# Kernel tuning notes

Hardware: AMD Instinct MI355X
Metric: run time of the kernel (lower is better)

## Reference

```python
import jax, jax.numpy as jnp
import numpy as np

EMBED = 1024
HEADS = 16
DIM_HEAD = EMBED // HEADS
N, L = 4, 2048


def setup_inputs() -> dict:
    key = jax.random.key(0)
    ks = jax.random.split(key, 12)
    s = 0.02
    return {
        "q": jax.random.normal(ks[0], (N, L, EMBED), jnp.float32),
        "k": jax.random.normal(ks[1], (N, L, EMBED), jnp.float32),
        "v": jax.random.normal(ks[2], (N, L, EMBED), jnp.float32),
        "padding_mask": jnp.ones((N, L), dtype=bool),
        "sequence_mask": jnp.zeros((L, L), dtype=bool),
        # Linear(in, out): store weight as [out, in] like torch, bias [out]
        "Wq": jax.random.normal(ks[3], (EMBED, EMBED), jnp.float32) * s,
        "bq": jnp.zeros((EMBED,), jnp.float32),
        "Wk": jax.random.normal(ks[4], (EMBED, EMBED), jnp.float32) * s,
        "bk": jnp.zeros((EMBED,), jnp.float32),
        "Wv": jax.random.normal(ks[5], (EMBED, EMBED), jnp.float32) * s,
        "bv": jnp.zeros((EMBED,), jnp.float32),
        "Wo": jax.random.normal(ks[6], (EMBED, EMBED), jnp.float32) * s,
        "bo": jnp.zeros((EMBED,), jnp.float32),
    }


def reference(q, k, v, padding_mask, sequence_mask, Wq, bq, Wk, bk, Wv, bv, Wo, bo):
    n, lq, _ = q.shape
    lk = k.shape[1]
    # input projections
    qp = (q @ Wq.T + bq).reshape(n, lq, HEADS, DIM_HEAD)
    kp = (k @ Wk.T + bk).reshape(n, lk, HEADS, DIM_HEAD)
    vp = (v @ Wv.T + bv).reshape(n, lk, HEADS, DIM_HEAD)
    # energy: [n, h, lq, lk]
    energy = jnp.einsum('nqhd,nkhd->nhqk', qp, kp)
    attention = jax.nn.softmax(energy / jnp.sqrt(jnp.float32(EMBED)), axis=3)
    # NOTE: the original torch code calls masked_fill (non in-place) and
    # discards the result, so padding_mask / sequence_mask have NO effect.
    # Dropout is also never applied in forward. Replicated faithfully.
    out = jnp.einsum('nhqk,nkhd->nqhd', attention, vp)
    out = out.reshape(n, lq, EMBED)
    return out @ Wo.T + bo
```

## Files before the change

### kernel.cpp

```cpp
#include <hip/hip_runtime.h>
#include <stdint.h>

typedef _Float16 f16;
typedef _Float16 f16x8 __attribute__((ext_vector_type(8)));
typedef _Float16 f16x4 __attribute__((ext_vector_type(4)));
typedef _Float16 f16x2 __attribute__((ext_vector_type(2)));
typedef __fp16 h16x2 __attribute__((ext_vector_type(2)));
typedef float f32x4 __attribute__((ext_vector_type(4)));

__device__ __forceinline__ f32x4 mfma16(f16x8 a, f16x8 b, f32x4 c) {
    return __builtin_amdgcn_mfma_f32_16x16x32_f16(a, b, c, 0, 0, 0);
}

__device__ __forceinline__ void gload16(const f16* g, f16* l) {
    __builtin_amdgcn_global_load_lds(
        (const __attribute__((address_space(1))) uint32_t*)g,
        (__attribute__((address_space(3))) uint32_t*)l, 16, 0, 0);
}

template <bool OUT16, bool BIASROW, bool XN>
__global__ __launch_bounds__(256, 2) void gemm128h(const f16* __restrict__ A,
                                                   const f16* __restrict__ B,
                                                   const float* __restrict__ bias,
                                                   void* __restrict__ Cout, long ldo) {
    __shared__ __align__(16) f16 As[128 * 64];
    __shared__ __align__(16) f16 Bs[128 * 64];
    int tid = threadIdx.x;
    int lane = tid & 63, w = tid >> 6;
    int wm = w & 1, wn = w >> 1;
    int l15 = lane & 15, quad = lane >> 4;
    long m0 = (long)(XN ? blockIdx.y : blockIdx.x) * 128;
    long n0 = (long)(XN ? blockIdx.x : blockIdx.y) * 128;

    int rg = lane >> 3;
    int cg = (lane & 7) ^ rg;
    const f16* ag[4];
    const f16* bg[4];
    f16* al[4];
    f16* bl[4];
#pragma unroll
    for (int t = 0; t < 4; ++t) {
        int rb = (w * 4 + t) * 8;
        ag[t] = A + (m0 + rb + rg) * 1024 + cg * 8;
        bg[t] = B + (n0 + rb + rg) * 1024 + cg * 8;
        al[t] = &As[rb * 64];
        bl[t] = &Bs[rb * 64];
    }

    f32x4 acc[4][4] = {};

    for (int k0 = 0; k0 < 1024; k0 += 64) {
        __syncthreads();
#pragma unroll
        for (int t = 0; t < 4; ++t) {
            gload16(ag[t] + k0, al[t]);
            gload16(bg[t] + k0, bl[t]);
        }
        __syncthreads();
#pragma unroll
        for (int ks = 0; ks < 2; ++ks) {
            int cc = (ks * 4 + quad) ^ (l15 & 7);
            f16x8 af[4], bf[4];
#pragma unroll
            for (int t = 0; t < 4; ++t) {
                af[t] = *(const f16x8*)&As[(wm * 64 + t * 16 + l15) * 64 + cc * 8];
                bf[t] = *(const f16x8*)&Bs[(wn * 64 + t * 16 + l15) * 64 + cc * 8];
            }
#pragma unroll
            for (int i = 0; i < 4; ++i)
#pragma unroll
                for (int j = 0; j < 4; ++j)
                    acc[i][j] = mfma16(af[i], bf[j], acc[i][j]);
        }
    }

#pragma unroll
    for (int i = 0; i < 4; ++i) {
        int mrow = wm * 64 + i * 16 + quad * 4;
#pragma unroll
        for (int j = 0; j < 4; ++j) {
            int ncol = wn * 64 + j * 16 + l15;
            long gn = n0 + ncol;
#pragma unroll
            for (int r = 0; r < 4; ++r) {
                long gm = m0 + mrow + r;
                float v = acc[i][j][r] + (BIASROW ? bias[gm] : bias[gn]);
                if constexpr (OUT16)
                    ((f16*)Cout)[gm * ldo + gn] = (f16)v;
                else
                    ((float*)Cout)[gm * ldo + gn] = v;
            }
        }
    }
}

__global__ __launch_bounds__(256, 2) void attn128(const f16* __restrict__ Qp,
                                                  const f16* __restrict__ Kp,
                                                  const f16* __restrict__ Vt,
                                                  f16* __restrict__ Op) {
    __shared__ __align__(16) f16 Qs[128 * 64];
    __shared__ __align__(16) f16 Ks[2][64 * 64];
    __shared__ __align__(16) f16 Vs[2][64 * 64];
    __shared__ __align__(16) f16 Ps[128 * 64];
    __shared__ float lsi[128];

    int tid = threadIdx.x;
    int lane = tid & 63, w = tid >> 6;
    int l15 = lane & 15, quad = lane >> 4;
    int b = blockIdx.x;
    int xcd = b & 7, slot = b >> 3;
    int nh = xcd * 8 + (slot >> 4);
    int qt = slot & 15;
    int nb = nh >> 4, h = nh & 15;
    long tok0 = (long)nb * 2048;

    int rg = lane >> 3, cg = (lane & 7) ^ rg;

    const f16* qsrc = Qp + (tok0 + qt * 128) * 1024 + h * 64;
#pragma unroll
    for (int t = 0; t < 4; ++t) {
        int rb = w * 32 + t * 8;
        gload16(qsrc + (rb + rg) * 1024 + cg * 8, &Qs[rb * 64]);
    }
    const f16* kbase = Kp + (tok0 + w * 16 + rg) * 1024 + h * 64 + cg * 8;
    const f16* vbase = Vt + ((long)h * 64 + w * 16 + rg) * 8192 + tok0 + cg * 8;
#pragma unroll
    for (int t = 0; t < 2; ++t) {
        gload16(kbase + t * 8 * 1024, &Ks[0][(w * 16 + t * 8) * 64]);
        gload16(vbase + (long)t * 8 * 8192, &Vs[0][(w * 16 + t * 8) * 64]);
    }
    __syncthreads();

    f16x8 qf[2][2];
#pragma unroll
    for (int ks = 0; ks < 2; ++ks) {
        int cc = (ks * 4 + quad) ^ (l15 & 7);
#pragma unroll
        for (int j = 0; j < 2; ++j)
            qf[ks][j] = *(const f16x8*)&Qs[(w * 32 + j * 16 + l15) * 64 + cc * 8];
    }

    f32x4 oacc[2][4] = {};
    float rsum[2] = {0.f, 0.f};

    for (int kt = 0; kt < 32; ++kt) {
        int cur = kt & 1;
        f32x4 sacc[4][2] = {};
#pragma unroll
        for (int ks = 0; ks < 2; ++ks) {
            int cc = (ks * 4 + quad) ^ (l15 & 7);
            f16x8 af[4];
#pragma unroll
            for (int t = 0; t < 4; ++t)
                af[t] = *(const f16x8*)&Ks[cur][(t * 16 + l15) * 64 + cc * 8];
#pragma unroll
            for (int i = 0; i < 4; ++i)
#pragma unroll
                for (int j = 0; j < 2; ++j)
                    sacc[i][j] = mfma16(af[i], qf[ks][j], sacc[i][j]);
        }
        if (kt < 31) {
            int nxt = cur ^ 1;
            const f16* kp2 = kbase + (long)(kt + 1) * 65536;
            const f16* vp2 = vbase + (kt + 1) * 64;
#pragma unroll
            for (int t = 0; t < 2; ++t) {
                gload16(kp2 + t * 8 * 1024, &Ks[nxt][(w * 16 + t * 8) * 64]);
                gload16(vp2 + (long)t * 8 * 8192, &Vs[nxt][(w * 16 + t * 8) * 64]);
            }
        }
#pragma unroll
        for (int i = 0; i < 4; ++i) {
#pragma unroll
            for (int j = 0; j < 2; ++j) {
                float p0 = __expf(sacc[i][j][0] * 0.03125f);
                float p1 = __expf(sacc[i][j][1] * 0.03125f);
                float p2 = __expf(sacc[i][j][2] * 0.03125f);
                float p3 = __expf(sacc[i][j][3] * 0.03125f);
                rsum[j] += (p0 + p1) + (p2 + p3);
                f16x2 lo = __builtin_bit_cast(f16x2, __builtin_amdgcn_cvt_pkrtz(p0, p1));
                f16x2 hi = __builtin_bit_cast(f16x2, __builtin_amdgcn_cvt_pkrtz(p2, p3));
                f16x4 ph;
                ph[0] = lo[0]; ph[1] = lo[1]; ph[2] = hi[0]; ph[3] = hi[1];
                int qrow = w * 32 + j * 16 + l15;
                int kl = i * 16 + quad * 4;
                int c = kl >> 3;
                *(f16x4*)&Ps[qrow * 64 + ((c ^ (qrow & 7)) << 3) + (kl & 7)] = ph;
            }
        }
        __syncthreads();
#pragma unroll
        for (int ks = 0; ks < 2; ++ks) {
            int cc = (ks * 4 + quad) ^ (l15 & 7);
            f16x8 af[2], bf[4];
#pragma unroll
            for (int i = 0; i < 2; ++i)
                af[i] = *(const f16x8*)&Ps[(w * 32 + i * 16 + l15) * 64 + cc * 8];
#pragma unroll
            for (int j = 0; j < 4; ++j)
                bf[j] = *(const f16x8*)&Vs[cur][(j * 16 + l15) * 64 + cc * 8];
#pragma unroll
            for (int i = 0; i < 2; ++i)
#pragma unroll
                for (int j = 0; j < 4; ++j)
                    oacc[i][j] = mfma16(af[i], bf[j], oacc[i][j]);
        }
        __syncthreads();
    }

#pragma unroll
    for (int j = 0; j < 2; ++j) {
        rsum[j] += __shfl_xor(rsum[j], 16, 64);
        rsum[j] += __shfl_xor(rsum[j], 32, 64);
    }
    if (lane < 16) {
        lsi[w * 32 + lane] = 1.0f / rsum[0];
        lsi[w * 32 + 16 + lane] = 1.0f / rsum[1];
    }
    __syncthreads();

    long otok = tok0 + (long)qt * 128;
#pragma unroll
    for (int i = 0; i < 2; ++i) {
        int qrow = w * 32 + i * 16 + quad * 4;
#pragma unroll
        for (int j = 0; j < 4; ++j) {
            int d = j * 16 + l15;
#pragma unroll
            for (int r = 0; r < 4; ++r) {
                float v = oacc[i][j][r] * lsi[qrow + r];
                Op[(otok + qrow + r) * 1024 + h * 64 + d] = (f16)v;
            }
        }
    }
}

__global__ void cvt_all(const float* __restrict__ q, const float* __restrict__ k,
                        const float* __restrict__ v, const float* __restrict__ w0,
                        const float* __restrict__ w1, const float* __restrict__ w2,
                        const float* __restrict__ w3, f16* __restrict__ qh,
                        f16* __restrict__ kh, f16* __restrict__ vh,
                        f16* __restrict__ wh) {
    long id = (long)blockIdx.x * 256 + threadIdx.x;
    const float* s;
    f16* d;
    long off;
    if (id < 3145728) {
        int which = (int)(id >> 20);
        off = (id & 1048575) * 8;
        s = which == 0 ? q : which == 1 ? k : v;
        d = which == 0 ? qh : which == 1 ? kh : vh;
    } else {
        long id2 = id - 3145728;
        int wi = (int)(id2 >> 17);
        off = (id2 & 131071) * 8;
        s = wi == 0 ? w0 : wi == 1 ? w1 : wi == 2 ? w2 : w3;
        d = wh + (long)wi * 1048576;
    }
    f32x4 a = *(const f32x4*)(s + off);
    f32x4 b = *(const f32x4*)(s + off + 4);
    f16x8 hv;
    hv[0] = (f16)a[0]; hv[1] = (f16)a[1]; hv[2] = (f16)a[2]; hv[3] = (f16)a[3];
    hv[4] = (f16)b[0]; hv[5] = (f16)b[1]; hv[6] = (f16)b[2]; hv[7] = (f16)b[3];
    *(f16x8*)(d + off) = hv;
}

extern "C" void kernel_launch(void* const* d_in, const int* in_sizes, int n_in,
                              void* d_out, int out_size, void* d_ws, size_t ws_size,
                              hipStream_t stream) {
    const float* q  = (const float*)d_in[0];
    const float* k  = (const float*)d_in[1];
    const float* v  = (const float*)d_in[2];
    const float* Wq = (const float*)d_in[5];
    const float* bq = (const float*)d_in[6];
    const float* Wk = (const float*)d_in[7];
    const float* bk = (const float*)d_in[8];
    const float* Wv = (const float*)d_in[9];
    const float* bv = (const float*)d_in[10];
    const float* Wo = (const float*)d_in[11];
    const float* bo = (const float*)d_in[12];

    char* ws = (char*)d_ws;
    f16* X  = (f16*)ws;
    f16* Wh = (f16*)(ws + (16L << 20));
    f16* Qp = (f16*)(ws + (24L << 20));
    f16* Kp = (f16*)(ws + (40L << 20));
    f16* Vt = (f16*)(ws + (56L << 20));
    f16* qh = Kp;
    f16* kh = Vt;
    f16* vh = X;
    f16* Op = X;

    cvt_all<<<14336, 256, 0, stream>>>(q, k, v, Wq, Wk, Wv, Wo, qh, kh, vh, Wh);

    gemm128h<true, false, false><<<dim3(64, 8), 256, 0, stream>>>(qh, Wh, bq, Qp, 1024);
    gemm128h<true, false, false><<<dim3(64, 8), 256, 0, stream>>>(kh, Wh + 1048576, bk, Kp, 1024);
    gemm128h<true, true, true><<<dim3(64, 8), 256, 0, stream>>>(Wh + 2097152, vh, bv, Vt, 8192);

    attn128<<<1024, 256, 0, stream>>>(Qp, Kp, Vt, Op);

    gemm128h<false, false, false><<<dim3(64, 8), 256, 0, stream>>>(Op, Wh + 3145728, bo, (float*)d_out, 1024);
}
```

Before: 343.2 us.

## Fuse QKV projections into one launch, fold softmax scale into Q, trim attention syncs

Merges the three Q/K/V projection GEMMs into a single launch that picks its operands by blockIdx.z, and moves the GEMM core into a shared device function. The Q projection now pre-multiplies by log2(e)/sqrt(1024), so attention can use exp2 directly without a per-element multiply. The attention kernel reuses the Q shared buffer for P and drops the block barrier between writing and reading P, since each warp touches only its own rows; the barrier before the final normalisation is also removed. These cut LDS use and raise the launch-bound occupancy hints. The workspace layout is reorganised to non-aliased buffers, which needs more workspace memory than before.

```diff
diff --git a/kernel.cpp b/kernel.cpp
--- a/kernel.cpp
+++ b/kernel.cpp
@@ -5,7 +5,6 @@
 typedef _Float16 f16x8 __attribute__((ext_vector_type(8)));
 typedef _Float16 f16x4 __attribute__((ext_vector_type(4)));
 typedef _Float16 f16x2 __attribute__((ext_vector_type(2)));
-typedef __fp16 h16x2 __attribute__((ext_vector_type(2)));
 typedef float f32x4 __attribute__((ext_vector_type(4)));
 
 __device__ __forceinline__ f32x4 mfma16(f16x8 a, f16x8 b, f32x4 c) {
@@ -18,19 +17,17 @@
         (__attribute__((address_space(3))) uint32_t*)l, 16, 0, 0);
 }
 
-template <bool OUT16, bool BIASROW, bool XN>
-__global__ __launch_bounds__(256, 2) void gemm128h(const f16* __restrict__ A,
-                                                   const f16* __restrict__ B,
-                                                   const float* __restrict__ bias,
-                                                   void* __restrict__ Cout, long ldo) {
-    __shared__ __align__(16) f16 As[128 * 64];
-    __shared__ __align__(16) f16 Bs[128 * 64];
+template <bool OUT16>
+__device__ __forceinline__ void gemm_body(const f16* __restrict__ A,
+                                          const f16* __restrict__ B,
+                                          const float* __restrict__ bias,
+                                          void* __restrict__ Cout, long ldo,
+                                          int biasrow, float scale,
+                                          long m0, long n0, f16* As, f16* Bs) {
     int tid = threadIdx.x;
     int lane = tid & 63, w = tid >> 6;
     int wm = w & 1, wn = w >> 1;
     int l15 = lane & 15, quad = lane >> 4;
-    long m0 = (long)(XN ? blockIdx.y : blockIdx.x) * 128;
-    long n0 = (long)(XN ? blockIdx.x : blockIdx.y) * 128;
 
     int rg = lane >> 3;
     int cg = (lane & 7) ^ rg;
@@ -84,7 +81,7 @@
 #pragma unroll
             for (int r = 0; r < 4; ++r) {
                 long gm = m0 + mrow + r;
-                float v = acc[i][j][r] + (BIASROW ? bias[gm] : bias[gn]);
+                float v = (acc[i][j][r] + (biasrow ? bias[gm] : bias[gn])) * scale;
                 if constexpr (OUT16)
                     ((f16*)Cout)[gm * ldo + gn] = (f16)v;
                 else
@@ -94,14 +91,54 @@
     }
 }
 
-__global__ __launch_bounds__(256, 2) void attn128(const f16* __restrict__ Qp,
+__global__ __launch_bounds__(256, 4) void qkv_proj(
+    const f16* __restrict__ qh, const f16* __restrict__ kh,
+    const f16* __restrict__ vh, const f16* __restrict__ Wh,
+    const float* __restrict__ bq, const float* __restrict__ bk,
+    const float* __restrict__ bv, f16* __restrict__ Qp, f16* __restrict__ Kp,
+    f16* __restrict__ Vt) {
+    __shared__ __align__(16) f16 As[128 * 64];
+    __shared__ __align__(16) f16 Bs[128 * 64];
+    int z = blockIdx.z;
+    const f16* A;
+    const f16* B;
+    const float* bias;
+    f16* C;
+    long ldo;
+    int biasrow;
+    float scale;
+    if (z == 0) {
+        A = qh; B = Wh; bias = bq; C = Qp; ldo = 1024; biasrow = 0;
+        scale = 0.0450842200277786f;
+    } else if (z == 1) {
+        A = kh; B = Wh + 1048576; bias = bk; C = Kp; ldo = 1024; biasrow = 0;
+        scale = 1.0f;
+    } else {
+        A = Wh + 2097152; B = vh; bias = bv; C = Vt; ldo = 8192; biasrow = 1;
+        scale = 1.0f;
+    }
+    long m0 = (long)(z == 2 ? blockIdx.y : blockIdx.x) * 128;
+    long n0 = (long)(z == 2 ? blockIdx.x : blockIdx.y) * 128;
+    gemm_body<true>(A, B, bias, C, ldo, biasrow, scale, m0, n0, As, Bs);
+}
+
+__global__ __launch_bounds__(256, 4) void o_proj(const f16* __restrict__ Op,
+                                                 const f16* __restrict__ Wo,
+                                                 const float* __restrict__ bo,
+                                                 float* __restrict__ out) {
+    __shared__ __align__(16) f16 As[128 * 64];
+    __shared__ __align__(16) f16 Bs[128 * 64];
+    gemm_body<false>(Op, Wo, bo, out, 1024, 0, 1.0f, (long)blockIdx.x * 128,
+                     (long)blockIdx.y * 128, As, Bs);
+}
+
+__global__ __launch_bounds__(256, 3) void attn128(const f16* __restrict__ Qp,
                                                   const f16* __restrict__ Kp,
                                                   const f16* __restrict__ Vt,
                                                   f16* __restrict__ Op) {
-    __shared__ __align__(16) f16 Qs[128 * 64];
+    __shared__ __align__(16) f16 QPs[128 * 64];
     __shared__ __align__(16) f16 Ks[2][64 * 64];
     __shared__ __align__(16) f16 Vs[2][64 * 64];
-    __shared__ __align__(16) f16 Ps[128 * 64];
     __shared__ float lsi[128];
 
     int tid = threadIdx.x;
@@ -120,15 +157,16 @@
 #pragma unroll
     for (int t = 0; t < 4; ++t) {
         int rb = w * 32 + t * 8;
-        gload16(qsrc + (rb + rg) * 1024 + cg * 8, &Qs[rb * 64]);
-    }
-    const f16* kbase = Kp + (tok0 + w * 16 + rg) * 1024 + h * 64 + cg * 8;
-    const f16* vbase = Vt + ((long)h * 64 + w * 16 + rg) * 8192 + tok0 + cg * 8;
-#pragma unroll
-    for (int t = 0; t < 2; ++t) {
-        gload16(kbase + t * 8 * 1024, &Ks[0][(w * 16 + t * 8) * 64]);
-        gload16(vbase + (long)t * 8 * 8192, &Vs[0][(w * 16 + t * 8) * 64]);
-    }
+        gload16(qsrc + (rb + rg) * 1024 + cg * 8, &QPs[rb * 64]);
+    }
+    const f16* kptr = Kp + (tok0 + w * 16 + rg) * 1024 + h * 64 + cg * 8;
+    const f16* vptr = Vt + ((long)h * 64 + w * 16 + rg) * 8192 + tok0 + cg * 8;
+    gload16(kptr, &Ks[0][(w * 16) * 64]);
+    gload16(kptr + 8 * 1024, &Ks[0][(w * 16 + 8) * 64]);
+    gload16(vptr, &Vs[0][(w * 16) * 64]);
+    gload16(vptr + (long)8 * 8192, &Vs[0][(w * 16 + 8) * 64]);
+    const f16* kn = kptr + 65536;
+    const f16* vn = vptr + 64;
     __syncthreads();
 
     f16x8 qf[2][2];
@@ -137,46 +175,52 @@
         int cc = (ks * 4 + quad) ^ (l15 & 7);
 #pragma unroll
         for (int j = 0; j < 2; ++j)
-            qf[ks][j] = *(const f16x8*)&Qs[(w * 32 + j * 16 + l15) * 64 + cc * 8];
+            qf[ks][j] = *(const f16x8*)&QPs[(w * 32 + j * 16 + l15) * 64 + cc * 8];
     }
 
     f32x4 oacc[2][4] = {};
     float rsum[2] = {0.f, 0.f};
+    const f32x4 z4 = {0.f, 0.f, 0.f, 0.f};
 
     for (int kt = 0; kt < 32; ++kt) {
         int cur = kt & 1;
-        f32x4 sacc[4][2] = {};
-#pragma unroll
-        for (int ks = 0; ks < 2; ++ks) {
-            int cc = (ks * 4 + quad) ^ (l15 & 7);
-            f16x8 af[4];
-#pragma unroll
-            for (int t = 0; t < 4; ++t)
-                af[t] = *(const f16x8*)&Ks[cur][(t * 16 + l15) * 64 + cc * 8];
+        f32x4 sacc[4][2];
+        {
+            int cc0 = quad ^ (l15 & 7);
+            int cc1 = (4 + quad) ^ (l15 & 7);
+            f16x8 a0[4], a1[4];
+#pragma unroll
+            for (int t = 0; t < 4; ++t) {
+                a0[t] = *(const f16x8*)&Ks[cur][(t * 16 + l15) * 64 + cc0 * 8];
+                a1[t] = *(const f16x8*)&Ks[cur][(t * 16 + l15) * 64 + cc1 * 8];
+            }
 #pragma unroll
             for (int i = 0; i < 4; ++i)
 #pragma unroll
-                for (int j = 0; j < 2; ++j)
-                    sacc[i][j] = mfma16(af[i], qf[ks][j], sacc[i][j]);
+                for (int j = 0; j < 2; ++j) {
+                    sacc[i][j] = mfma16(a0[i], qf[0][j], z4);
+                    sacc[i][j] = mfma16(a1[i], qf[1][j], sacc[i][j]);
+                }
         }
         if (kt < 31) {
             int nxt = cur ^ 1;
-            const f16* kp2 = kbase + (long)(kt + 1) * 65536;
-            const f16* vp2 = vbase + (kt + 1) * 64;
-#pragma unroll
-            for (int t = 0; t < 2; ++t) {
-                gload16(kp2 + t * 8 * 1024, &Ks[nxt][(w * 16 + t * 8) * 64]);
-                gload16(vp2 + (long)t * 8 * 8192, &Vs[nxt][(w * 16 + t * 8) * 64]);
-            }
+            f16* kd = &Ks[nxt][(w * 16) * 64];
+            f16* vd = &Vs[nxt][(w * 16) * 64];
+            gload16(kn, kd);
+            gload16(kn + 8 * 1024, kd + 8 * 64);
+            gload16(vn, vd);
+            gload16(vn + (long)8 * 8192, vd + 8 * 64);
+            kn += 65536;
+            vn += 64;
         }
 #pragma unroll
         for (int i = 0; i < 4; ++i) {
 #pragma unroll
             for (int j = 0; j < 2; ++j) {
-                float p0 = __expf(sacc[i][j][0] * 0.03125f);
-                float p1 = __expf(sacc[i][j][1] * 0.03125f);
-                float p2 = __expf(sacc[i][j][2] * 0.03125f);
-                float p3 = __expf(sacc[i][j][3] * 0.03125f);
+                float p0 = __builtin_exp2f(sacc[i][j][0]);
+                float p1 = __builtin_exp2f(sacc[i][j][1]);
+                float p2 = __builtin_exp2f(sacc[i][j][2]);
+                float p3 = __builtin_exp2f(sacc[i][j][3]);
                 rsum[j] += (p0 + p1) + (p2 + p3);
                 f16x2 lo = __builtin_bit_cast(f16x2, __builtin_amdgcn_cvt_pkrtz(p0, p1));
                 f16x2 hi = __builtin_bit_cast(f16x2, __builtin_amdgcn_cvt_pkrtz(p2, p3));
@@ -185,17 +229,16 @@
                 int qrow = w * 32 + j * 16 + l15;
                 int kl = i * 16 + quad * 4;
                 int c = kl >> 3;
-                *(f16x4*)&Ps[qrow * 64 + ((c ^ (qrow & 7)) << 3) + (kl & 7)] = ph;
-            }
-        }
-        __syncthreads();
+                *(f16x4*)&QPs[qrow * 64 + ((c ^ (qrow & 7)) << 3) + (kl & 7)] = ph;
+            }
+        }
 #pragma unroll
         for (int ks = 0; ks < 2; ++ks) {
             int cc = (ks * 4 + quad) ^ (l15 & 7);
             f16x8 af[2], bf[4];
 #pragma unroll
             for (int i = 0; i < 2; ++i)
-                af[i] = *(const f16x8*)&Ps[(w * 32 + i * 16 + l15) * 64 + cc * 8];
+                af[i] = *(const f16x8*)&QPs[(w * 32 + i * 16 + l15) * 64 + cc * 8];
 #pragma unroll
             for (int j = 0; j < 4; ++j)
                 bf[j] = *(const f16x8*)&Vs[cur][(j * 16 + l15) * 64 + cc * 8];
@@ -217,7 +260,6 @@
         lsi[w * 32 + lane] = 1.0f / rsum[0];
         lsi[w * 32 + 16 + lane] = 1.0f / rsum[1];
     }
-    __syncthreads();
 
     long otok = tok0 + (long)qt * 128;
 #pragma unroll
@@ -281,23 +323,21 @@
     const float* bo = (const float*)d_in[12];
 
     char* ws = (char*)d_ws;
-    f16* X  = (f16*)ws;
-    f16* Wh = (f16*)(ws + (16L << 20));
-    f16* Qp = (f16*)(ws + (24L << 20));
-    f16* Kp = (f16*)(ws + (40L << 20));
-    f16* Vt = (f16*)(ws + (56L << 20));
-    f16* qh = Kp;
-    f16* kh = Vt;
-    f16* vh = X;
-    f16* Op = X;
+    f16* qh = (f16*)ws;
+    f16* kh = (f16*)(ws + (16L << 20));
+    f16* vh = (f16*)(ws + (32L << 20));
+    f16* Wh = (f16*)(ws + (48L << 20));
+    f16* Qp = (f16*)(ws + (56L << 20));
+    f16* Kp = (f16*)(ws + (72L << 20));
+    f16* Vt = (f16*)(ws + (88L << 20));
+    f16* Op = (f16*)(ws + (104L << 20));
 
     cvt_all<<<14336, 256, 0, stream>>>(q, k, v, Wq, Wk, Wv, Wo, qh, kh, vh, Wh);
 
-    gemm128h<true, false, false><<<dim3(64, 8), 256, 0, stream>>>(qh, Wh, bq, Qp, 1024);
-    gemm128h<true, false, false><<<dim3(64, 8), 256, 0, stream>>>(kh, Wh + 1048576, bk, Kp, 1024);
-    gemm128h<true, true, true><<<dim3(64, 8), 256, 0, stream>>>(Wh + 2097152, vh, bv, Vt, 8192);
+    qkv_proj<<<dim3(64, 8, 3), 256, 0, stream>>>(qh, kh, vh, Wh, bq, bk, bv,
+                                                 Qp, Kp, Vt);
 
     attn128<<<1024, 256, 0, stream>>>(Qp, Kp, Vt, Op);
 
-    gemm128h<false, false, false><<<dim3(64, 8), 256, 0, stream>>>(Op, Wh + 3145728, bo, (float*)d_out, 1024);
-}
+    o_proj<<<dim3(64, 8), 256, 0, stream>>>(Op, Wh + 3145728, bo, (float*)d_out);
+}
```

After: 406.8 us. 18.5% more time.
